# Kernel tuning notes

Hardware: AMD Instinct MI355X
Metric: run time of the kernel (lower is better)

Reference implementation:

```python
import jax, jax.numpy as jnp
import numpy as np
import math

N = 100000      # n_entities
C = 128         # channel
E = 600000      # n_edges
NNZ = 1000000   # interact_mat nnz
NU = 50000      # n_users
NREL = 25       # n_relations
H = 4           # n_heads
DK = C // H     # d_k


def setup_inputs() -> dict:
    key = jax.random.key(0)
    ks = jax.random.split(key, 13)
    s = 1.0 / math.sqrt(C)
    return {
        "entity_emb": jax.random.normal(ks[0], (N, C), jnp.float32),
        "W_Q": jax.random.normal(ks[1], (C, C), jnp.float32) * s,
        "W_K": jax.random.normal(ks[2], (C, C), jnp.float32) * s,
        "W_V": jax.random.normal(ks[3], (C, C), jnp.float32) * s,
        "W_O": jax.random.normal(ks[4], (C, C), jnp.float32) * s,
        "relation_att": jax.random.normal(ks[5], (NREL - 1, H, DK, DK), jnp.float32) * s,
        "relation_msg": jax.random.normal(ks[6], (NREL - 1, H, DK, DK), jnp.float32) * s,
        "relation_emb": jax.random.normal(ks[7], (NREL - 1, C), jnp.float32),
        "edge_index": jax.random.randint(ks[8], (2, E), 0, N, jnp.int32),
        "edge_type": jax.random.randint(ks[9], (E,), 1, NREL, jnp.int32),
        "im_rows": jax.random.randint(ks[10], (NNZ,), 0, NU, jnp.int32),
        "im_cols": jax.random.randint(ks[11], (NNZ,), 0, N, jnp.int32),
        "im_vals": jax.random.uniform(ks[12], (NNZ,), jnp.float32),
        "n_users": NU,
    }


def reference(entity_emb, W_Q, W_K, W_V, W_O, relation_att, relation_msg,
              relation_emb, edge_index, edge_type, im_rows, im_cols, im_vals,
              n_users):
    n_entities, channel = entity_emb.shape
    n_heads, d_k = H, channel // H
    head, tail = edge_index[0], edge_index[1]
    rel = edge_type - 1

    # Step 1: heterogeneous mutual attention
    q = (entity_emb[head] @ W_Q).reshape(-1, n_heads, d_k)            # [E,H,Dk]
    k = (entity_emb[tail] @ W_K).reshape(-1, n_heads, d_k)
    k = jnp.einsum("ehd,ehdk->ehk", k, relation_att[rel])
    score = (q * k).sum(-1) / math.sqrt(d_k)                           # [E,H]

    # Step 2: heterogeneous message passing
    v = (entity_emb[tail] @ W_V).reshape(-1, n_heads, d_k)
    v = jnp.einsum("ehd,ehdk->ehk", v, relation_msg[rel])

    # scatter_softmax over target node id (head)
    seg_max = jax.ops.segment_max(score, head, num_segments=n_entities)  # [N,H]
    ex = jnp.exp(score - seg_max[head])
    denom = jax.ops.segment_sum(ex, head, num_segments=n_entities)
    attn = ex / denom[head]                                              # [E,H]

    agg = (v * attn[..., None]).reshape(-1, n_heads * d_k) @ W_O         # [E,C]
    entity_agg = jax.ops.segment_sum(agg, head, num_segments=n_entities)

    # user aggregate: sparse [NU,N] @ entity_emb
    user_agg = jax.ops.segment_sum(entity_emb[im_cols] * im_vals[:, None],
                                   im_rows, num_segments=n_users)
    return entity_agg, user_agg
```

## Files before the change

kernel.cpp:

```cpp
#include <hip/hip_runtime.h>
#include <hip/hip_bf16.h>
#include <math.h>

typedef __attribute__((ext_vector_type(8))) unsigned short u16x8;
typedef __attribute__((ext_vector_type(4))) unsigned short u16x4;
typedef __attribute__((ext_vector_type(8))) short bf16x8;
typedef __attribute__((ext_vector_type(4))) float f32x4;

#define NRELMAX 32

__device__ __forceinline__ float b2f(unsigned short u) {
    return __uint_as_float(((unsigned)u) << 16);
}
__device__ __forceinline__ unsigned short f2b(float v) {
    __hip_bfloat16 b = __float2bfloat16(v);
    return *reinterpret_cast<unsigned short*>(&b);
}

__device__ __forceinline__ bf16x8 lda_frag(const __hip_bfloat16* p) {
    return *(const bf16x8*)p;
}
__device__ __forceinline__ void st_o(__hip_bfloat16* p, float v) { *p = __float2bfloat16(v); }
__device__ __forceinline__ void st_o(float* p, float v) { *p = v; }

template <typename TO>
__device__ __forceinline__ void gemm_body(const __hip_bfloat16* __restrict__ A,
                                          const __hip_bfloat16* __restrict__ Wt,
                                          TO* __restrict__ out, int n, int blk)
{
    const int tid = threadIdx.x;
    const int w = tid >> 6;
    const int l = tid & 63;
    const int q = l >> 4;
    const int c16 = l & 15;
    const int wr = (w >> 1) * 64;
    const int wc = (w & 1) * 64;
    const long row0 = (long)blk * 128;

    f32x4 acc[4][4] = {};
    #pragma unroll
    for (int ks = 0; ks < 4; ++ks) {
        bf16x8 af[4];
        #pragma unroll
        for (int rb = 0; rb < 4; ++rb) {
            long r = row0 + wr + rb * 16 + c16;
            if (r >= n) r = n - 1;
            af[rb] = lda_frag(A + r * 128 + ks * 32 + q * 8);
        }
        #pragma unroll
        for (int cb = 0; cb < 4; ++cb) {
            bf16x8 wf = *(const bf16x8*)(Wt + (size_t)(wc + cb * 16 + c16) * 128 + ks * 32 + q * 8);
            #pragma unroll
            for (int rb = 0; rb < 4; ++rb)
                acc[rb][cb] = __builtin_amdgcn_mfma_f32_16x16x32_bf16(af[rb], wf, acc[rb][cb], 0, 0, 0);
        }
    }
    #pragma unroll
    for (int rb = 0; rb < 4; ++rb) {
        #pragma unroll
        for (int r = 0; r < 4; ++r) {
            long row = row0 + wr + rb * 16 + q * 4 + r;
            if (row < n) {
                #pragma unroll
                for (int cb = 0; cb < 4; ++cb)
                    st_o(out + row * 128 + wc + cb * 16 + c16, acc[rb][cb][r]);
            }
        }
    }
}

template <typename TO>
__global__ __launch_bounds__(256) void mfma_gemm(const __hip_bfloat16* __restrict__ A,
                                                 const __hip_bfloat16* __restrict__ Wt,
                                                 TO* __restrict__ out, int n)
{
    gemm_body<TO>(A, Wt, out, n, blockIdx.x);
}

__global__ __launch_bounds__(256) void prep(
    const float* __restrict__ W0, const float* __restrict__ W1,
    const float* __restrict__ W2, const float* __restrict__ W3,
    __hip_bfloat16* __restrict__ T0, __hip_bfloat16* __restrict__ T1,
    __hip_bfloat16* __restrict__ T2, __hip_bfloat16* __restrict__ T3,
    const float* __restrict__ att, const float* __restrict__ msg,
    __hip_bfloat16* __restrict__ Atab, __hip_bfloat16* __restrict__ Mtab, int nrel,
    const float* __restrict__ emb, __hip_bfloat16* __restrict__ embb, long n4,
    int nbW, int nbT)
{
    const int tid = threadIdx.x;
    const int bx = blockIdx.x;
    if (bx < nbW) {
        int t = bx * 256 + tid;
        int w = t >> 14, r = t & 16383;
        const float* W = (w == 0) ? W0 : (w == 1) ? W1 : (w == 2) ? W2 : W3;
        __hip_bfloat16* T = (w == 0) ? T0 : (w == 1) ? T1 : (w == 2) ? T2 : T3;
        int k = r >> 7, c = r & 127;
        T[(size_t)c * 128 + k] = __float2bfloat16(W[(size_t)k * 128 + c]);
        return;
    }
    if (bx < nbW + nbT) {
        int t = (bx - nbW) * 256 + tid;
        int tot = nrel * 4096;
        if (t >= 2 * tot) return;
        const float* src = (t < tot) ? att : msg;
        __hip_bfloat16* dst = (t < tot) ? Atab : Mtab;
        int u = (t < tot) ? t : t - tot;
        int rel = u >> 12, rem = u & 4095;
        int h = rem >> 10;  rem &= 1023;
        int s2 = rem >> 9;  rem &= 511;
        int lane = rem >> 3, j = rem & 7;
        int g = lane >> 4, c = lane & 15;
        dst[u] = __float2bfloat16(src[(size_t)rel * 4096 + h * 1024 + s2 * 16 + (g * 8 + j) * 32 + c]);
        return;
    }
    long i = ((long)(bx - nbW - nbT) * 256 + tid) * 4;
    if (i >= n4 * 4) return;
    float4 v = *(const float4*)(emb + i);
    u16x4 o;
    o[0] = f2b(v.x); o[1] = f2b(v.y); o[2] = f2b(v.z); o[3] = f2b(v.w);
    *(u16x4*)(embb + i) = o;
}

__global__ __launch_bounds__(256) void qkv_count(
    const int* __restrict__ head, const int* __restrict__ etyp,
    const int* __restrict__ irow,
    unsigned* __restrict__ ecnt, unsigned* __restrict__ ucnt,
    unsigned* __restrict__ rcnt, int* __restrict__ plocalE,
    int* __restrict__ plocalU, int E, int NNZ, int nbX,
    const __hip_bfloat16* __restrict__ A,
    const __hip_bfloat16* __restrict__ WtQ, const __hip_bfloat16* __restrict__ WtK,
    const __hip_bfloat16* __restrict__ WtV,
    __hip_bfloat16* __restrict__ Qb, __hip_bfloat16* __restrict__ Kb,
    __hip_bfloat16* __restrict__ Vb, int n, int gg)
{
    __shared__ unsigned lcnt[NRELMAX];
    const int tid = threadIdx.x;
    const int bx = blockIdx.x;
    if (bx < nbX) {
        if (tid < NRELMAX) lcnt[tid] = 0;
        __syncthreads();
        int i = bx * 256 + tid;
        if (i < E) {
            unsigned p = atomicAdd(&ecnt[head[i]], 1u);
            plocalE[i] = (int)p;
            atomicAdd(&lcnt[etyp[i] - 1], 1u);
        }
        if (i < NNZ) {
            unsigned p = atomicAdd(&ucnt[irow[i]], 1u);
            plocalU[i] = (int)p;
        }
        __syncthreads();
        if (tid < NRELMAX) {
            unsigned c = lcnt[tid];
            if (c) atomicAdd(&rcnt[tid], c);
        }
        return;
    }
    int b2 = bx - nbX;
    int which = b2 / gg;
    int blk = b2 % gg;
    const __hip_bfloat16* Wt = (which == 0) ? WtQ : (which == 1) ? WtK : WtV;
    __hip_bfloat16* Out = (which == 0) ? Qb : (which == 1) ? Kb : Vb;
    gemm_body<__hip_bfloat16>(A, Wt, Out, n, blk);
}

__global__ __launch_bounds__(1024) void scan_p1(
    unsigned* __restrict__ ecnt, int n_e, unsigned* __restrict__ bsumE,
    unsigned* __restrict__ ucnt, int n_u, unsigned* __restrict__ bsumU, int nbE)
{
    unsigned* buf; unsigned* bsum; int n; int blk;
    if ((int)blockIdx.x < nbE) { buf = ecnt; bsum = bsumE; n = n_e; blk = blockIdx.x; }
    else { buf = ucnt; bsum = bsumU; n = n_u; blk = blockIdx.x - nbE; }
    __shared__ unsigned sh[1024];
    int i = blk * 1024 + threadIdx.x;
    unsigned v = (i < n) ? buf[i] : 0u;
    sh[threadIdx.x] = v;
    __syncthreads();
    for (int off = 1; off < 1024; off <<= 1) {
        unsigned t = (threadIdx.x >= (unsigned)off) ? sh[threadIdx.x - off] : 0u;
        __syncthreads();
        sh[threadIdx.x] += t;
        __syncthreads();
    }
    if (i < n) buf[i] = sh[threadIdx.x] - v;
    if (threadIdx.x == 1023) bsum[blk] = sh[1023];
}

__global__ __launch_bounds__(1024) void scan_p2(
    unsigned* __restrict__ bsumE, int nbE, unsigned* __restrict__ bsumU, int nbU,
    const unsigned* __restrict__ rcnt, unsigned* __restrict__ rcur,
    unsigned* __restrict__ rend, unsigned* __restrict__ rnext, int nrel)
{
    if (blockIdx.x == 2) {
        if (threadIdx.x == 0) {
            unsigned acc = 0;
            for (int r = 0; r < nrel; ++r) {
                rcur[r] = acc;
                rend[r] = acc + rcnt[r];
                acc += (rcnt[r] + 15u) & ~15u;
                rnext[r] = acc;
            }
        }
        return;
    }
    unsigned* bsum = (blockIdx.x == 0) ? bsumE : bsumU;
    int nb = (blockIdx.x == 0) ? nbE : nbU;
    __shared__ unsigned sh[1024];
    unsigned v = (threadIdx.x < (unsigned)nb) ? bsum[threadIdx.x] : 0u;
    sh[threadIdx.x] = v;
    __syncthreads();
    for (int off = 1; off < 1024; off <<= 1) {
        unsigned t = (threadIdx.x >= (unsigned)off) ? sh[threadIdx.x - off] : 0u;
        __syncthreads();
        sh[threadIdx.x] += t;
        __syncthreads();
    }
    if (threadIdx.x < (unsigned)nb) bsum[threadIdx.x] = sh[threadIdx.x] - v;
}

__global__ __launch_bounds__(1024) void scan_p3(
    unsigned* __restrict__ ecnt, int n_e, const unsigned* __restrict__ bsumE,
    unsigned* __restrict__ ucnt, int n_u, const unsigned* __restrict__ bsumU, int nbE)
{
    unsigned* buf; const unsigned* bsum; int n; int blk;
    if ((int)blockIdx.x < nbE) { buf = ecnt; bsum = bsumE; n = n_e; blk = blockIdx.x; }
    else { buf = ucnt; bsum = bsumU; n = n_u; blk = blockIdx.x - nbE; }
    int i = blk * 1024 + threadIdx.x;
    if (i < n) buf[i] += bsum[blk];
}

__global__ __launch_bounds__(256) void fills(
    const int* __restrict__ irow, const int* __restrict__ icol,
    const float* __restrict__ ival, const unsigned* __restrict__ ustart,
    const int* __restrict__ plocalU, int2* __restrict__ upair, int NNZ,
    const int* __restrict__ head, const int* __restrict__ tail,
    const int* __restrict__ etyp, const unsigned* __restrict__ estart,
    const int* __restrict__ plocalE, unsigned* __restrict__ rcur,
    int4* __restrict__ emeta, int E,
    const unsigned* __restrict__ rend, const unsigned* __restrict__ rnext,
    int nrel, long emax, int nbU, int nbE)
{
    __shared__ unsigned lcnt[NRELMAX];
    __shared__ unsigned lbase[NRELMAX];
    const int tid = threadIdx.x;
    const int bx = blockIdx.x;
    if (bx < nbU) {
        int i = bx * 256 + tid;
        if (i < NNZ) {
            unsigned slot = ustart[irow[i]] + (unsigned)plocalU[i];
            upair[slot] = make_int2(icol[i], __float_as_int(ival[i]));
        }
        return;
    }
    if (bx < nbU + nbE) {
        if (tid < NRELMAX) lcnt[tid] = 0;
        __syncthreads();
        int i = (bx - nbU) * 256 + tid;
        int r = 0;
        unsigned lpos = 0;
        if (i < E) {
            r = etyp[i] - 1;
            lpos = atomicAdd(&lcnt[r], 1u);
        }
        __syncthreads();
        if (tid < NRELMAX) {
            unsigned c = lcnt[tid];
            lbase[tid] = c ? atomicAdd(&rcur[tid], c) : 0u;
        }
        __syncthreads();
        if (i < E) {
            int hn = head[i];
            unsigned slot = estart[hn] + (unsigned)plocalE[i];
            emeta[lbase[r] + lpos] = make_int4(hn, tail[i], (int)slot, r);
        }
        return;
    }
    for (int r = 0; r < nrel; ++r) {
        unsigned s = rend[r], e2 = rnext[r];
        for (unsigned i = s + tid; i < e2; i += 256)
            emeta[i] = make_int4(0, 0, -1, r);
    }
    long ep = rnext[nrel - 1];
    for (long i = ep + tid; i < emax; i += 256)
        emeta[i] = make_int4(0, 0, -1, nrel - 1);
}

template <int ROUND>
__global__ __launch_bounds__(256, 4) void edge_pass(
    const __hip_bfloat16* __restrict__ Qb, const __hip_bfloat16* __restrict__ Kb,
    const __hip_bfloat16* __restrict__ Vb,
    const __hip_bfloat16* __restrict__ Atab, const __hip_bfloat16* __restrict__ Mtab,
    const int4* __restrict__ emeta, float* __restrict__ SC,
    __hip_bfloat16* __restrict__ VPh, long Epad, int chunk)
{
    const int wv = (blockIdx.x * 256 + threadIdx.x) >> 6;
    const int l = threadIdx.x & 63;
    const int g = l >> 4;
    const int c = l & 15;
    long j0 = (long)wv * chunk;
    if (j0 >= Epad) return;
    long j1 = j0 + chunk; if (j1 > Epad) j1 = Epad;

    bf16x8 aK[2][2], aM[2][2];
    int currel = -1;
    for (long pos = j0; pos < j1; pos += 16) {
        const int4 md = emeta[pos + c];
        const int rel0 = __shfl(md.w, 0, 64);
        if (rel0 != currel) {
            currel = rel0;
            #pragma unroll
            for (int hl = 0; hl < 2; ++hl) {
                const int h = ROUND * 2 + hl;
                #pragma unroll
                for (int s2 = 0; s2 < 2; ++s2) {
                    size_t idx = ((((size_t)rel0 * 4 + h) * 2 + s2) * 64 + l) * 8;
                    aK[hl][s2] = *(const bf16x8*)(Atab + idx);
                    aM[hl][s2] = *(const bf16x8*)(Mtab + idx);
                }
            }
        }
        const int tn = md.y, hn = md.x, slot = md.z;
        #pragma unroll
        for (int hl = 0; hl < 2; ++hl) {
            const int h = ROUND * 2 + hl;
            bf16x8 bk = *(const bf16x8*)(Kb + (size_t)tn * 128 + h * 32 + g * 8);
            bf16x8 bv = *(const bf16x8*)(Vb + (size_t)tn * 128 + h * 32 + g * 8);
            f32x4 z = {0.f, 0.f, 0.f, 0.f};
            f32x4 klo = __builtin_amdgcn_mfma_f32_16x16x32_bf16(aK[hl][0], bk, z, 0, 0, 0);
            f32x4 khi = __builtin_amdgcn_mfma_f32_16x16x32_bf16(aK[hl][1], bk, z, 0, 0, 0);
            f32x4 vlo = __builtin_amdgcn_mfma_f32_16x16x32_bf16(aM[hl][0], bv, z, 0, 0, 0);
            f32x4 vhi = __builtin_amdgcn_mfma_f32_16x16x32_bf16(aM[hl][1], bv, z, 0, 0, 0);
            const __hip_bfloat16* qp = Qb + (size_t)hn * 128 + h * 32;
            u16x4 q1 = *(const u16x4*)(qp + g * 4);
            u16x4 q2 = *(const u16x4*)(qp + 16 + g * 4);
            float p = 0.f;
            #pragma unroll
            for (int r = 0; r < 4; ++r)
                p += b2f(q1[r]) * klo[r] + b2f(q2[r]) * khi[r];
            p += __shfl_xor(p, 16, 64);
            p += __shfl_xor(p, 32, 64);
            if (slot >= 0) {
                if (g == 0) SC[(size_t)slot * 4 + h] = p * 0.17677669529663687f;
                u16x4 plo, phi;
                #pragma unroll
                for (int r = 0; r < 4; ++r) { plo[r] = f2b(vlo[r]); phi[r] = f2b(vhi[r]); }
                __hip_bfloat16* dst = VPh + (size_t)slot * 64 + hl * 32;
                *(u16x4*)(dst + g * 4) = plo;
                *(u16x4*)(dst + 16 + g * 4) = phi;
            }
        }
    }
}

template <int ROUND>
__global__ __launch_bounds__(256) void node_pass(
    const float* __restrict__ SC, const __hip_bfloat16* __restrict__ VPh,
    const unsigned* __restrict__ estart, __hip_bfloat16* __restrict__ M, int n, int Etot)
{
    int node = (blockIdx.x * 256 + threadIdx.x) >> 6;
    if (node >= n) return;
    int l = threadIdx.x & 63;
    int half = l >> 5;
    const int h = ROUND * 2 + half;
    unsigned beg = estart[node];
    unsigned end = (node + 1 < n) ? estart[node + 1] : (unsigned)Etot;
    float mx = -INFINITY, dn = 0.f;
    for (unsigned j = beg; j < end; ++j) {
        float s = SC[(size_t)j * 4 + h];
        float m2 = fmaxf(mx, s);
        dn = dn * __expf(mx - m2) + __expf(s - m2);
        mx = m2;
    }
    float inv = (end > beg) ? 1.f / dn : 0.f;
    float acc = 0.f;
    for (unsigned j = beg; j < end; ++j) {
        float w = __expf(SC[(size_t)j * 4 + h] - mx) * inv;
        acc = fmaf(w, __bfloat162float(VPh[(size_t)j * 64 + l]), acc);
    }
    M[(size_t)node * 128 + ROUND * 64 + l] = __float2bfloat16(acc);
}

__global__ __launch_bounds__(256) void user_gather(
    const __hip_bfloat16* __restrict__ embb, const unsigned* __restrict__ ustart,
    const int2* __restrict__ upair, float* __restrict__ out, int nu, int NNZ)
{
    int u = (blockIdx.x * 256 + threadIdx.x) >> 5;
    if (u >= nu) return;
    int l = threadIdx.x & 31;
    unsigned beg = ustart[u];
    unsigned end = (u + 1 < nu) ? ustart[u + 1] : (unsigned)NNZ;
    float a0 = 0.f, a1 = 0.f, a2 = 0.f, a3 = 0.f;
    float b0 = 0.f, b1 = 0.f, b2 = 0.f, b3 = 0.f;
    unsigned j = beg;
    for (; j + 3 < end; j += 4) {
        int2 p0 = upair[j], p1 = upair[j + 1], p2 = upair[j + 2], p3 = upair[j + 3];
        float v0 = __int_as_float(p0.y), v1 = __int_as_float(p1.y);
        float v2 = __int_as_float(p2.y), v3 = __int_as_float(p3.y);
        uint2 e0 = *(const uint2*)((const unsigned*)(embb + (size_t)p0.x * 128) + l * 2);
        uint2 e1 = *(const uint2*)((const unsigned*)(embb + (size_t)p1.x * 128) + l * 2);
        uint2 e2 = *(const uint2*)((const unsigned*)(embb + (size_t)p2.x * 128) + l * 2);
        uint2 e3 = *(const uint2*)((const unsigned*)(embb + (size_t)p3.x * 128) + l * 2);
        a0 = fmaf(b2f((unsigned short)(e0.x & 0xFFFF)), v0, a0);
        a1 = fmaf(b2f((unsigned short)(e0.x >> 16)), v0, a1);
        a2 = fmaf(b2f((unsigned short)(e0.y & 0xFFFF)), v0, a2);
        a3 = fmaf(b2f((unsigned short)(e0.y >> 16)), v0, a3);
        b0 = fmaf(b2f((unsigned short)(e1.x & 0xFFFF)), v1, b0);
        b1 = fmaf(b2f((unsigned short)(e1.x >> 16)), v1, b1);
        b2 = fmaf(b2f((unsigned short)(e1.y & 0xFFFF)), v1, b2);
        b3 = fmaf(b2f((unsigned short)(e1.y >> 16)), v1, b3);
        a0 = fmaf(b2f((unsigned short)(e2.x & 0xFFFF)), v2, a0);
        a1 = fmaf(b2f((unsigned short)(e2.x >> 16)), v2, a1);
        a2 = fmaf(b2f((unsigned short)(e2.y & 0xFFFF)), v2, a2);
        a3 = fmaf(b2f((unsigned short)(e2.y >> 16)), v2, a3);
        b0 = fmaf(b2f((unsigned short)(e3.x & 0xFFFF)), v3, b0);
        b1 = fmaf(b2f((unsigned short)(e3.x >> 16)), v3, b1);
        b2 = fmaf(b2f((unsigned short)(e3.y & 0xFFFF)), v3, b2);
        b3 = fmaf(b2f((unsigned short)(e3.y >> 16)), v3, b3);
    }
    for (; j < end; ++j) {
        int2 p0 = upair[j];
        float v0 = __int_as_float(p0.y);
        uint2 e0 = *(const uint2*)((const unsigned*)(embb + (size_t)p0.x * 128) + l * 2);
        a0 = fmaf(b2f((unsigned short)(e0.x & 0xFFFF)), v0, a0);
        a1 = fmaf(b2f((unsigned short)(e0.x >> 16)), v0, a1);
        a2 = fmaf(b2f((unsigned short)(e0.y & 0xFFFF)), v0, a2);
        a3 = fmaf(b2f((unsigned short)(e0.y >> 16)), v0, a3);
    }
    *(float4*)(out + (size_t)u * 128 + l * 4) =
        make_float4(a0 + b0, a1 + b1, a2 + b2, a3 + b3);
}

extern "C" void kernel_launch(void* const* d_in, const int* in_sizes, int n_in,
                              void* d_out, int out_size, void* d_ws, size_t ws_size,
                              hipStream_t stream)
{
    const float* emb = (const float*)d_in[0];
    const float* W_Q = (const float*)d_in[1];
    const float* W_K = (const float*)d_in[2];
    const float* W_V = (const float*)d_in[3];
    const float* W_O = (const float*)d_in[4];
    const float* att = (const float*)d_in[5];
    const float* msg = (const float*)d_in[6];
    const int* eidx  = (const int*)d_in[8];
    const int* etyp  = (const int*)d_in[9];
    const int* irow  = (const int*)d_in[10];
    const int* icol  = (const int*)d_in[11];
    const float* ival = (const float*)d_in[12];

    const int N    = in_sizes[0] / 128;
    const int E    = in_sizes[8] / 2;
    const int NNZ  = in_sizes[10];
    const int NU   = out_size / 128 - N;
    const int NREL = in_sizes[5] / 4096;

    const int* head = eidx;
    const int* tail = eidx + E;

    const int NUp = (NU + 255) & ~255;

    const size_t NC = (size_t)N * 128;
    char* p = (char*)d_ws;
    __hip_bfloat16* VPh = (__hip_bfloat16*)p; p += (size_t)E * 64 * 2;
    __hip_bfloat16* Kb  = (__hip_bfloat16*)p; p += NC * 2;
    __hip_bfloat16* Vb  = (__hip_bfloat16*)p; p += NC * 2;
    __hip_bfloat16* M   = (__hip_bfloat16*)p; p += NC * 2;
    unsigned* rcnt  = (unsigned*)p; p += 32 * 4;
    unsigned* rcur  = (unsigned*)p; p += 32 * 4;
    unsigned* rend  = (unsigned*)p; p += 32 * 4;
    unsigned* rnext = (unsigned*)p; p += 32 * 4;
    unsigned* ucnt  = (unsigned*)p; p += (size_t)NUp * 4;
    unsigned* bsumE = (unsigned*)p; p += 1024 * 4;
    unsigned* bsumU = (unsigned*)p; p += 1024 * 4;
    int2* upair     = (int2*)p;     p += (size_t)NNZ * 8;
    __hip_bfloat16* WtQ = (__hip_bfloat16*)p; p += 16384 * 2;
    __hip_bfloat16* WtK = (__hip_bfloat16*)p; p += 16384 * 2;
    __hip_bfloat16* WtV = (__hip_bfloat16*)p; p += 16384 * 2;
    __hip_bfloat16* WtO = (__hip_bfloat16*)p; p += 16384 * 2;
    __hip_bfloat16* Atab = (__hip_bfloat16*)p; p += (size_t)NREL * 4096 * 2;
    __hip_bfloat16* Mtab = (__hip_bfloat16*)p; p += (size_t)NREL * 4096 * 2;

    int* plocalU = (int*)VPh;
    int* plocalE = plocalU + NNZ;

    float* out_ent = (float*)d_out;
    float* out_usr = out_ent + NC;
    __hip_bfloat16* embb = (__hip_bfloat16*)out_ent;
    __hip_bfloat16* Qb   = (__hip_bfloat16*)((char*)d_out + NC * 2);
    const long Emax = E + 512;
    float* SC   = out_usr;
    int4* emeta = (int4*)(out_usr + (size_t)E * 4);
    unsigned* ecnt = (unsigned*)((char*)emeta + (size_t)Emax * 16);

    hipMemsetAsync(rcnt, 0, (32 * 4) * 4 + (size_t)NUp * 4, stream);
    hipMemsetAsync(ecnt, 0, (size_t)N * 4, stream);

    const int nbW = 256;
    const int nbT = (2 * NREL * 4096 + 255) / 256;
    const int nbC = (int)((NC / 4 + 255) / 256);
    prep<<<nbW + nbT + nbC, 256, 0, stream>>>(
        W_Q, W_K, W_V, W_O, WtQ, WtK, WtV, WtO,
        att, msg, Atab, Mtab, NREL,
        emb, embb, (long)(NC / 4), nbW, nbT);

    int gg = (N + 127) / 128;
    const int nbX = ((NNZ > E ? NNZ : E) + 255) / 256;
    qkv_count<<<nbX + 3 * gg, 256, 0, stream>>>(
        head, etyp, irow, ecnt, ucnt, rcnt, plocalE, plocalU, E, NNZ, nbX,
        embb, WtQ, WtK, WtV, Qb, Kb, Vb, N, gg);

    int nbE2 = (N + 1023) / 1024;
    int nbU2 = (NU + 1023) / 1024;
    scan_p1<<<nbE2 + nbU2, 1024, 0, stream>>>(ecnt, N, bsumE, ucnt, NU, bsumU, nbE2);
    scan_p2<<<3, 1024, 0, stream>>>(bsumE, nbE2, bsumU, nbU2, rcnt, rcur, rend, rnext, NREL);
    scan_p3<<<nbE2 + nbU2, 1024, 0, stream>>>(ecnt, N, bsumE, ucnt, NU, bsumU, nbE2);

    const int nbU = (NNZ + 255) / 256;
    const int nbE = (E + 255) / 256;
    fills<<<nbU + nbE + 1, 256, 0, stream>>>(
        irow, icol, ival, ucnt, plocalU, upair, NNZ,
        head, tail, etyp, ecnt, plocalE, rcur, emeta, E,
        rend, rnext, NREL, Emax, nbU, nbE);

    const int NWAVE = 16384;
    int chunk = (int)(((Emax + NWAVE - 1) / NWAVE + 15) & ~15L);
    edge_pass<0><<<NWAVE / 4, 256, 0, stream>>>(Qb, Kb, Vb, Atab, Mtab, emeta, SC, VPh, Emax, chunk);
    node_pass<0><<<(N + 3) / 4, 256, 0, stream>>>(SC, VPh, ecnt, M, N, E);
    edge_pass<1><<<NWAVE / 4, 256, 0, stream>>>(Qb, Kb, Vb, Atab, Mtab, emeta, SC, VPh, Emax, chunk);
    node_pass<1><<<(N + 3) / 4, 256, 0, stream>>>(SC, VPh, ecnt, M, N, E);

    user_gather<<<(NU + 7) / 8, 256, 0, stream>>>(embb, ucnt, upair, out_usr, NU, NNZ);

    mfma_gemm<float><<<gg, 256, 0, stream>>>(M, WtO, out_ent, N);
}
```

Baseline: 583.9 us.

## Fuse user aggregation into edge passes, split users across the two rounds

Removes the standalone user_gather kernel and appends its blocks to the two edge_pass launches, each handling half of the users. The aim is to overlap the irregular user gather with the edge work and save a launch. The user gather now reads the fp32 input embeddings instead of the bf16 copy, which doubles the bytes gathered per row but improves accuracy. To free the user output region, the SC/emeta scratch moves into the dead bf16 embedding area of the entity output and ecnt moves into the workspace, so the two memsets become one.

After: 613.6 us. 5.1% more time.

```diff
diff --git a/kernel.cpp b/kernel.cpp
--- a/kernel.cpp
+++ b/kernel.cpp
@@ -286,13 +286,47 @@
 }
 
 template <int ROUND>
-__global__ __launch_bounds__(256, 4) void edge_pass(
+__global__ __launch_bounds__(256, 4) void edge_user(
     const __hip_bfloat16* __restrict__ Qb, const __hip_bfloat16* __restrict__ Kb,
     const __hip_bfloat16* __restrict__ Vb,
     const __hip_bfloat16* __restrict__ Atab, const __hip_bfloat16* __restrict__ Mtab,
     const int4* __restrict__ emeta, float* __restrict__ SC,
-    __hip_bfloat16* __restrict__ VPh, long Epad, int chunk)
-{
+    __hip_bfloat16* __restrict__ VPh, long Epad, int chunk, int EB,
+    const float* __restrict__ emb, const unsigned* __restrict__ ustart,
+    const int2* __restrict__ upair, float* __restrict__ uout,
+    int u0, int u1, int nu, int NNZ)
+{
+    if ((int)blockIdx.x >= EB) {
+        int ub = blockIdx.x - EB;
+        int u = u0 + ((ub * 256 + threadIdx.x) >> 5);
+        if (u >= u1) return;
+        int l = threadIdx.x & 31;
+        unsigned beg = ustart[u];
+        unsigned end = (u + 1 < nu) ? ustart[u + 1] : (unsigned)NNZ;
+        float4 A = make_float4(0.f, 0.f, 0.f, 0.f);
+        float4 B = make_float4(0.f, 0.f, 0.f, 0.f);
+        unsigned j = beg;
+        for (; j + 1 < end; j += 2) {
+            int2 p0 = upair[j], p1 = upair[j + 1];
+            float v0 = __int_as_float(p0.y), v1 = __int_as_float(p1.y);
+            float4 e0 = *(const float4*)(emb + (size_t)p0.x * 128 + l * 4);
+            float4 e1 = *(const float4*)(emb + (size_t)p1.x * 128 + l * 4);
+            A.x = fmaf(e0.x, v0, A.x); A.y = fmaf(e0.y, v0, A.y);
+            A.z = fmaf(e0.z, v0, A.z); A.w = fmaf(e0.w, v0, A.w);
+            B.x = fmaf(e1.x, v1, B.x); B.y = fmaf(e1.y, v1, B.y);
+            B.z = fmaf(e1.z, v1, B.z); B.w = fmaf(e1.w, v1, B.w);
+        }
+        if (j < end) {
+            int2 p0 = upair[j];
+            float v0 = __int_as_float(p0.y);
+            float4 e0 = *(const float4*)(emb + (size_t)p0.x * 128 + l * 4);
+            A.x = fmaf(e0.x, v0, A.x); A.y = fmaf(e0.y, v0, A.y);
+            A.z = fmaf(e0.z, v0, A.z); A.w = fmaf(e0.w, v0, A.w);
+        }
+        *(float4*)(uout + (size_t)u * 128 + l * 4) =
+            make_float4(A.x + B.x, A.y + B.y, A.z + B.z, A.w + B.w);
+        return;
+    }
     const int wv = (blockIdx.x * 256 + threadIdx.x) >> 6;
     const int l = threadIdx.x & 63;
     const int g = l >> 4;
@@ -380,56 +414,6 @@
     M[(size_t)node * 128 + ROUND * 64 + l] = __float2bfloat16(acc);
 }
 
-__global__ __launch_bounds__(256) void user_gather(
-    const __hip_bfloat16* __restrict__ embb, const unsigned* __restrict__ ustart,
-    const int2* __restrict__ upair, float* __restrict__ out, int nu, int NNZ)
-{
-    int u = (blockIdx.x * 256 + threadIdx.x) >> 5;
-    if (u >= nu) return;
-    int l = threadIdx.x & 31;
-    unsigned beg = ustart[u];
-    unsigned end = (u + 1 < nu) ? ustart[u + 1] : (unsigned)NNZ;
-    float a0 = 0.f, a1 = 0.f, a2 = 0.f, a3 = 0.f;
-    float b0 = 0.f, b1 = 0.f, b2 = 0.f, b3 = 0.f;
-    unsigned j = beg;
-    for (; j + 3 < end; j += 4) {
-        int2 p0 = upair[j], p1 = upair[j + 1], p2 = upair[j + 2], p3 = upair[j + 3];
-        float v0 = __int_as_float(p0.y), v1 = __int_as_float(p1.y);
-        float v2 = __int_as_float(p2.y), v3 = __int_as_float(p3.y);
-        uint2 e0 = *(const uint2*)((const unsigned*)(embb + (size_t)p0.x * 128) + l * 2);
-        uint2 e1 = *(const uint2*)((const unsigned*)(embb + (size_t)p1.x * 128) + l * 2);
-        uint2 e2 = *(const uint2*)((const unsigned*)(embb + (size_t)p2.x * 128) + l * 2);
-        uint2 e3 = *(const uint2*)((const unsigned*)(embb + (size_t)p3.x * 128) + l * 2);
-        a0 = fmaf(b2f((unsigned short)(e0.x & 0xFFFF)), v0, a0);
-        a1 = fmaf(b2f((unsigned short)(e0.x >> 16)), v0, a1);
-        a2 = fmaf(b2f((unsigned short)(e0.y & 0xFFFF)), v0, a2);
-        a3 = fmaf(b2f((unsigned short)(e0.y >> 16)), v0, a3);
-        b0 = fmaf(b2f((unsigned short)(e1.x & 0xFFFF)), v1, b0);
-        b1 = fmaf(b2f((unsigned short)(e1.x >> 16)), v1, b1);
-        b2 = fmaf(b2f((unsigned short)(e1.y & 0xFFFF)), v1, b2);
-        b3 = fmaf(b2f((unsigned short)(e1.y >> 16)), v1, b3);
-        a0 = fmaf(b2f((unsigned short)(e2.x & 0xFFFF)), v2, a0);
-        a1 = fmaf(b2f((unsigned short)(e2.x >> 16)), v2, a1);
-        a2 = fmaf(b2f((unsigned short)(e2.y & 0xFFFF)), v2, a2);
-        a3 = fmaf(b2f((unsigned short)(e2.y >> 16)), v2, a3);
-        b0 = fmaf(b2f((unsigned short)(e3.x & 0xFFFF)), v3, b0);
-        b1 = fmaf(b2f((unsigned short)(e3.x >> 16)), v3, b1);
-        b2 = fmaf(b2f((unsigned short)(e3.y & 0xFFFF)), v3, b2);
-        b3 = fmaf(b2f((unsigned short)(e3.y >> 16)), v3, b3);
-    }
-    for (; j < end; ++j) {
-        int2 p0 = upair[j];
-        float v0 = __int_as_float(p0.y);
-        uint2 e0 = *(const uint2*)((const unsigned*)(embb + (size_t)p0.x * 128) + l * 2);
-        a0 = fmaf(b2f((unsigned short)(e0.x & 0xFFFF)), v0, a0);
-        a1 = fmaf(b2f((unsigned short)(e0.x >> 16)), v0, a1);
-        a2 = fmaf(b2f((unsigned short)(e0.y & 0xFFFF)), v0, a2);
-        a3 = fmaf(b2f((unsigned short)(e0.y >> 16)), v0, a3);
-    }
-    *(float4*)(out + (size_t)u * 128 + l * 4) =
-        make_float4(a0 + b0, a1 + b1, a2 + b2, a3 + b3);
-}
-
 extern "C" void kernel_launch(void* const* d_in, const int* in_sizes, int n_in,
                               void* d_out, int out_size, void* d_ws, size_t ws_size,
                               hipStream_t stream)
@@ -469,6 +453,7 @@
     unsigned* rend  = (unsigned*)p; p += 32 * 4;
     unsigned* rnext = (unsigned*)p; p += 32 * 4;
     unsigned* ucnt  = (unsigned*)p; p += (size_t)NUp * 4;
+    unsigned* ecnt  = (unsigned*)p; p += (size_t)N * 4;
     unsigned* bsumE = (unsigned*)p; p += 1024 * 4;
     unsigned* bsumU = (unsigned*)p; p += 1024 * 4;
     int2* upair     = (int2*)p;     p += (size_t)NNZ * 8;
@@ -487,12 +472,10 @@
     __hip_bfloat16* embb = (__hip_bfloat16*)out_ent;
     __hip_bfloat16* Qb   = (__hip_bfloat16*)((char*)d_out + NC * 2);
     const long Emax = E + 512;
-    float* SC   = out_usr;
-    int4* emeta = (int4*)(out_usr + (size_t)E * 4);
-    unsigned* ecnt = (unsigned*)((char*)emeta + (size_t)Emax * 16);
-
-    hipMemsetAsync(rcnt, 0, (32 * 4) * 4 + (size_t)NUp * 4, stream);
-    hipMemsetAsync(ecnt, 0, (size_t)N * 4, stream);
+    float* SC   = (float*)d_out;
+    int4* emeta = (int4*)((char*)d_out + (size_t)E * 16);
+
+    hipMemsetAsync(rcnt, 0, (size_t)(4 * 32 * 4) + (size_t)NUp * 4 + (size_t)N * 4, stream);
 
     const int nbW = 256;
     const int nbT = (2 * NREL * 4096 + 255) / 256;
@@ -523,12 +506,18 @@
 
     const int NWAVE = 16384;
     int chunk = (int)(((Emax + NWAVE - 1) / NWAVE + 15) & ~15L);
-    edge_pass<0><<<NWAVE / 4, 256, 0, stream>>>(Qb, Kb, Vb, Atab, Mtab, emeta, SC, VPh, Emax, chunk);
+    const int EB = NWAVE / 4;
+    const int NU1 = (NU + 1) / 2;
+    const int ub0 = (NU1 + 7) / 8;
+    const int ub1 = (NU - NU1 + 7) / 8;
+    edge_user<0><<<EB + ub0, 256, 0, stream>>>(
+        Qb, Kb, Vb, Atab, Mtab, emeta, SC, VPh, Emax, chunk, EB,
+        emb, ucnt, upair, out_usr, 0, NU1, NU, NNZ);
     node_pass<0><<<(N + 3) / 4, 256, 0, stream>>>(SC, VPh, ecnt, M, N, E);
-    edge_pass<1><<<NWAVE / 4, 256, 0, stream>>>(Qb, Kb, Vb, Atab, Mtab, emeta, SC, VPh, Emax, chunk);
+    edge_user<1><<<EB + ub1, 256, 0, stream>>>(
+        Qb, Kb, Vb, Atab, Mtab, emeta, SC, VPh, Emax, chunk, EB,
+        emb, ucnt, upair, out_usr, NU1, NU, NU, NNZ);
     node_pass<1><<<(N + 3) / 4, 256, 0, stream>>>(SC, VPh, ecnt, M, N, E);
 
-    user_gather<<<(NU + 7) / 8, 256, 0, stream>>>(embb, ucnt, upair, out_usr, NU, NNZ);
-
     mfma_gemm<float><<<gg, 256, 0, stream>>>(M, WtO, out_ent, N);
 }
```
